# Kernel optimization log

Hardware: AMD Instinct MI355X
Metric: run time of the kernel (lower is better)

The kernel has to match this reference:

```python
import jax, jax.numpy as jnp
import numpy as np


def setup_inputs() -> dict:
    key = jax.random.key(0)
    ks = jax.random.split(key, 6)
    B, T, H, L, V = 8, 100, 1024, 512, 32000
    x = jax.random.normal(ks[0], (B, T, H), dtype=jnp.float32)
    attn_dist = jax.random.normal(ks[1], (B, T, L), dtype=jnp.float32)
    enc_input = jax.random.randint(ks[2], (B, L), 0, V, dtype=jnp.int32)
    W_vocab = jax.random.normal(ks[3], (H, V), dtype=jnp.float32) * (1.0 / np.sqrt(H))
    b_vocab = jnp.zeros((V,), dtype=jnp.float32)
    w_gen = jax.random.normal(ks[4], (H, 1), dtype=jnp.float32) * (1.0 / np.sqrt(H))
    b_gen = jnp.zeros((1,), dtype=jnp.float32)
    return {"x": x, "attn_dist": attn_dist, "enc_input": enc_input,
            "W_vocab": W_vocab, "b_vocab": b_vocab, "w_gen": w_gen, "b_gen": b_gen}


def reference(x, attn_dist, enc_input, W_vocab, b_vocab, w_gen, b_gen):
    B, T, H = x.shape
    L = attn_dist.shape[-1]
    V = W_vocab.shape[-1]
    # generation gate: sigmoid(x @ w_gen + b_gen) -> [B, T, 1]
    p_gen = jax.nn.sigmoid(jnp.einsum('bth,ho->bto', x, w_gen) + b_gen)
    # vocab distribution: softmax over vocab of the projection -> [B, T, V]
    vocab_dist = jax.nn.softmax(jnp.einsum('bth,hv->btv', x, W_vocab) + b_vocab, axis=-1)
    vocab_dist = p_gen * vocab_dist
    # copy distribution over encoder positions -> [B, T, L]
    copy_dist = (1.0 - p_gen) * jax.nn.softmax(attn_dist, axis=-1)
    # scatter-add copy probabilities into vocab slots (duplicates accumulate)
    vd = vocab_dist.reshape(B * T, V)
    cd = copy_dist.reshape(B * T, L)
    idx = jnp.broadcast_to(enc_input[:, None, :], (B, T, L)).reshape(B * T, L)
    rows = jnp.arange(B * T, dtype=jnp.int32)[:, None]
    combined = vd.at[rows, idx].add(cd)
    return jnp.log(combined).reshape(B, T, V)
```

## Files before the change

kernel.cpp:

```cpp
#include <hip/hip_runtime.h>
#include <math.h>

#define BB 8
#define TT 100
#define HH 1024
#define LL 512
#define VV 32000
#define NROWS (BB*TT)
#define MPAD 896
#define NMT 7
#define NNT 250
#define NWG (NMT*NNT)

typedef __bf16 bf16x8 __attribute__((ext_vector_type(8)));
typedef __bf16 bf16x4 __attribute__((ext_vector_type(4)));
typedef float f32x4 __attribute__((ext_vector_type(4)));

__device__ __forceinline__ void gload16(const void* g, void* l) {
  __builtin_amdgcn_global_load_lds(
      (const __attribute__((address_space(1))) unsigned int*)g,
      (__attribute__((address_space(3))) unsigned int*)l, 16, 0, 0);
}

__global__ __launch_bounds__(256) void k_cvt_x(const float* __restrict__ x,
                                               __bf16* __restrict__ xb) {
  int idx = blockIdx.x * 256 + threadIdx.x;
  int row = (idx * 4) >> 10;
  bf16x4 v;
  if (row < NROWS) {
    float4 f = ((const float4*)x)[idx];
    v[0] = (__bf16)f.x; v[1] = (__bf16)f.y; v[2] = (__bf16)f.z; v[3] = (__bf16)f.w;
  } else {
    v[0] = v[1] = v[2] = v[3] = (__bf16)0.f;
  }
  ((bf16x4*)xb)[idx] = v;
}

__global__ __launch_bounds__(256) void k_cvt_wT(const float* __restrict__ W,
                                                __bf16* __restrict__ Wtb) {
  __shared__ float T[32][257];
  int n0 = blockIdx.x * 256;
  int kt = blockIdx.y;
  int tid = threadIdx.x;
#pragma unroll
  for (int i = 0; i < 32; ++i)
    T[i][tid] = W[(size_t)(kt * 32 + i) * VV + n0 + tid];
  __syncthreads();
  int cq = tid & 3;
  int cl = tid >> 2;
  __bf16* base = Wtb + ((size_t)kt * VV + n0) * 32;
#pragma unroll
  for (int g = 0; g < 4; ++g) {
    int col = g * 64 + cl;
    bf16x8 v;
#pragma unroll
    for (int j = 0; j < 8; ++j) v[j] = (__bf16)T[cq * 8 + j][col];
    *(bf16x8*)(base + (size_t)col * 32 + cq * 8) = v;
  }
}

__global__ __launch_bounds__(256) void k_pgen_copy(
    const float* __restrict__ x, const float* __restrict__ attn,
    const float* __restrict__ w_gen, const float* __restrict__ b_gen,
    float* __restrict__ p_gen, float* __restrict__ copy_dist,
    float* __restrict__ rsum) {
  int r = blockIdx.x;
  int tid = threadIdx.x;
  __shared__ float red[4];
  if (tid == 0) rsum[r] = 0.f;

  float d = 0.f;
  for (int h = tid; h < HH; h += 256) d += x[(size_t)r * HH + h] * w_gen[h];
#pragma unroll
  for (int o = 32; o > 0; o >>= 1) d += __shfl_down(d, o, 64);
  if ((tid & 63) == 0) red[tid >> 6] = d;
  __syncthreads();
  float dot = red[0] + red[1] + red[2] + red[3];
  float p = 1.f / (1.f + __expf(-(dot + b_gen[0])));
  if (tid == 0) p_gen[r] = p;

  float a0 = attn[(size_t)r * LL + tid];
  float a1 = attn[(size_t)r * LL + 256 + tid];
  float m = fmaxf(a0, a1);
#pragma unroll
  for (int o = 32; o > 0; o >>= 1) m = fmaxf(m, __shfl_down(m, o, 64));
  __syncthreads();
  if ((tid & 63) == 0) red[tid >> 6] = m;
  __syncthreads();
  float M = fmaxf(fmaxf(red[0], red[1]), fmaxf(red[2], red[3]));
  float e0 = __expf(a0 - M), e1 = __expf(a1 - M);
  float s = e0 + e1;
#pragma unroll
  for (int o = 32; o > 0; o >>= 1) s += __shfl_down(s, o, 64);
  __syncthreads();
  if ((tid & 63) == 0) red[tid >> 6] = s;
  __syncthreads();
  float S = red[0] + red[1] + red[2] + red[3];
  float scale = (1.f - p) / S;
  copy_dist[(size_t)r * LL + tid] = e0 * scale;
  copy_dist[(size_t)r * LL + 256 + tid] = e1 * scale;
}

__global__ __launch_bounds__(256) void k_gemm_mfma(
    const __bf16* __restrict__ Xb, const __bf16* __restrict__ Wtb,
    const float* __restrict__ bias, float* __restrict__ out,
    float* __restrict__ rsum) {
  __shared__ __align__(16) __bf16 As[3][128 * 32];
  __shared__ __align__(16) __bf16 Bs[3][128 * 32];
  int tid = threadIdx.x;
  int lane = tid & 63, wave = tid >> 6;
  int wr = wave >> 1, wc = wave & 1;
  int l15 = lane & 15, quad = lane >> 4;

  int lid = blockIdx.x;
  int xcd = lid & 7, sub = lid >> 3;
  const int q = NWG >> 3, rr = NWG & 7;
  int wg = (xcd < rr) ? (xcd * (q + 1) + sub)
                      : (rr * (q + 1) + (xcd - rr) * q + sub);
  int m0 = (wg % NMT) * 128;
  int n0 = (wg / NMT) * 128;

  f32x4 acc[4][4];
#pragma unroll
  for (int mi = 0; mi < 4; ++mi)
#pragma unroll
    for (int ni = 0; ni < 4; ++ni) acc[mi][ni] = (f32x4){0.f, 0.f, 0.f, 0.f};

  int r0 = wave * 32;
  int lr = lane >> 2;
  int chunk = (lane & 3) ^ ((lr >> 1) & 3);
  const __bf16* aptr0 = Xb + (size_t)(m0 + r0 + lr) * HH + chunk * 8;
  const __bf16* aptr1 = aptr0 + (size_t)16 * HH;
  const size_t bstep = (size_t)VV * 32;
  const __bf16* bptr0 = Wtb + (size_t)(n0 + r0 + lr) * 32 + chunk * 8;
  const __bf16* bptr1 = bptr0 + (size_t)16 * 32;

  int sw8 = (quad ^ ((l15 >> 1) & 3)) * 8;

#define STAGE(it, buf) do {                                          \
    gload16(aptr0 + (size_t)(it) * 32, &As[buf][r0 * 32]);           \
    gload16(aptr1 + (size_t)(it) * 32, &As[buf][(r0 + 16) * 32]);    \
    gload16(bptr0 + (size_t)(it) * bstep, &Bs[buf][r0 * 32]);        \
    gload16(bptr1 + (size_t)(it) * bstep, &Bs[buf][(r0 + 16) * 32]); \
  } while (0)

#define SYNCW(n) do {                                          \
    asm volatile("s_waitcnt vmcnt(" #n ")" ::: "memory");      \
    __builtin_amdgcn_s_barrier();                              \
    __builtin_amdgcn_sched_barrier(0);                         \
  } while (0)

#define COMPUTE(buf) do {                                                     \
    const __bf16* Ab = As[buf];                                               \
    const __bf16* Bb = Bs[buf];                                               \
    bf16x8 af[4], bfg[4];                                                     \
    _Pragma("unroll")                                                         \
    for (int mi = 0; mi < 4; ++mi)                                            \
      af[mi] = *(const bf16x8*)&Ab[(wr * 64 + mi * 16 + l15) * 32 + sw8];     \
    _Pragma("unroll")                                                         \
    for (int ni = 0; ni < 4; ++ni)                                            \
      bfg[ni] = *(const bf16x8*)&Bb[(wc * 64 + ni * 16 + l15) * 32 + sw8];    \
    _Pragma("unroll")                                                         \
    for (int mi = 0; mi < 4; ++mi)                                            \
      _Pragma("unroll")                                                       \
      for (int ni = 0; ni < 4; ++ni)                                          \
        acc[mi][ni] = __builtin_amdgcn_mfma_f32_16x16x32_bf16(                \
            af[mi], bfg[ni], acc[mi][ni], 0, 0, 0);                           \
  } while (0)

  STAGE(0, 0);
  STAGE(1, 1);
  for (int itb = 0; itb < 30; itb += 3) {
    SYNCW(4); STAGE(itb + 2, 2); COMPUTE(0);
    SYNCW(4); STAGE(itb + 3, 0); COMPUTE(1);
    SYNCW(4); STAGE(itb + 4, 1); COMPUTE(2);
  }
  SYNCW(4);
  COMPUTE(0);
  SYNCW(0);
  COMPUTE(1);

  float bv4[4];
#pragma unroll
  for (int ni = 0; ni < 4; ++ni) bv4[ni] = bias[n0 + wc * 64 + ni * 16 + l15];

#pragma unroll
  for (int mi = 0; mi < 4; ++mi) {
#pragma unroll
    for (int rg = 0; rg < 4; ++rg) {
      int row = m0 + wr * 64 + mi * 16 + quad * 4 + rg;
      bool valid = row < NROWS;
      float esum = 0.f;
#pragma unroll
      for (int ni = 0; ni < 4; ++ni) {
        int col = n0 + wc * 64 + ni * 16 + l15;
        float v = acc[mi][ni][rg] + bv4[ni];
        if (valid) out[(size_t)row * VV + col] = v;
        esum += __expf(v);
      }
#pragma unroll
      for (int o = 8; o > 0; o >>= 1) esum += __shfl_down(esum, o, 16);
      if (l15 == 0 && valid) atomicAdd(&rsum[row], esum);
    }
  }
#undef STAGE
#undef SYNCW
#undef COMPUTE
}

__global__ __launch_bounds__(256) void k_affine_scatter(
    float* __restrict__ out, const float* __restrict__ p_gen,
    const float* __restrict__ rsum, const int* __restrict__ enc,
    const float* __restrict__ copy) {
  __shared__ int hkey[1024];
  __shared__ float hval[1024];
  int r = blockIdx.x, tid = threadIdx.x;
  float* row = out + (size_t)r * VV;
  float logc = __logf(p_gen[r] / rsum[r]);
  for (int i = tid; i < 1024; i += 256) { hkey[i] = -1; hval[i] = 0.f; }
  __syncthreads();
  int b = r / TT;
  for (int j = tid; j < LL; j += 256) {
    int v = enc[(size_t)b * LL + j];
    float cv = copy[(size_t)r * LL + j];
    unsigned h = ((unsigned)v * 2654435761u) & 1023u;
    while (true) {
      int prev = atomicCAS(&hkey[h], -1, v);
      if (prev == -1 || prev == v) { atomicAdd(&hval[h], cv); break; }
      h = (h + 1) & 1023u;
    }
  }
  for (int c4 = tid; c4 < VV / 4; c4 += 256) {
    float4 v = ((float4*)row)[c4];
    v.x += logc; v.y += logc; v.z += logc; v.w += logc;
    ((float4*)row)[c4] = v;
  }
  __syncthreads();
  for (int h = tid; h < 1024; h += 256) {
    int col = hkey[h];
    if (col >= 0) {
      float stored = row[col];
      row[col] = __logf(__expf(stored) + hval[h]);
    }
  }
}

extern "C" void kernel_launch(void* const* d_in, const int* in_sizes, int n_in,
                              void* d_out, int out_size, void* d_ws, size_t ws_size,
                              hipStream_t stream) {
  const float* x    = (const float*)d_in[0];
  const float* attn = (const float*)d_in[1];
  const int*   enc  = (const int*)d_in[2];
  const float* Wv   = (const float*)d_in[3];
  const float* bv   = (const float*)d_in[4];
  const float* wgen = (const float*)d_in[5];
  const float* bg   = (const float*)d_in[6];
  float* out = (float*)d_out;
  float* ws = (float*)d_ws;

  float* p_gen = ws;
  float* rsum  = ws + 1024;
  float* copy  = ws + 2048;
  __bf16* xb = (__bf16*)(ws + 2048 + NROWS * LL);
  __bf16* Wt = (__bf16*)((char*)xb + (size_t)MPAD * HH * 2);

  k_cvt_x<<<MPAD * HH / 4 / 256, 256, 0, stream>>>(x, xb);
  dim3 gw(VV / 256, HH / 32);
  k_cvt_wT<<<gw, 256, 0, stream>>>(Wv, Wt);
  k_pgen_copy<<<NROWS, 256, 0, stream>>>(x, attn, wgen, bg, p_gen, copy, rsum);
  k_gemm_mfma<<<NWG, 256, 0, stream>>>(xb, Wt, bv, out, rsum);
  k_affine_scatter<<<NROWS, 256, 0, stream>>>(out, p_gen, rsum, enc, copy);
}
```

Measured before the change: 405.9 us.

## Fuse W fp32-to-bf16 transpose into GEMM B-tile loading

Removes the separate kernel that converts and transposes W_vocab to bf16. The GEMM now loads fp32 W directly through registers, converts it and writes swizzled bf16 into LDS. The pipeline drops from three LDS buffers to two. This avoids a full extra read and write of the 128MB weight, but each of the 7 M-tiles now rereads fp32 W, doubling B bytes per tile, and loses the async direct-to-LDS path for B.

```diff
diff --git a/kernel.cpp b/kernel.cpp
--- a/kernel.cpp
+++ b/kernel.cpp
@@ -36,29 +36,6 @@
   ((bf16x4*)xb)[idx] = v;
 }
 
-__global__ __launch_bounds__(256) void k_cvt_wT(const float* __restrict__ W,
-                                                __bf16* __restrict__ Wtb) {
-  __shared__ float T[32][257];
-  int n0 = blockIdx.x * 256;
-  int kt = blockIdx.y;
-  int tid = threadIdx.x;
-#pragma unroll
-  for (int i = 0; i < 32; ++i)
-    T[i][tid] = W[(size_t)(kt * 32 + i) * VV + n0 + tid];
-  __syncthreads();
-  int cq = tid & 3;
-  int cl = tid >> 2;
-  __bf16* base = Wtb + ((size_t)kt * VV + n0) * 32;
-#pragma unroll
-  for (int g = 0; g < 4; ++g) {
-    int col = g * 64 + cl;
-    bf16x8 v;
-#pragma unroll
-    for (int j = 0; j < 8; ++j) v[j] = (__bf16)T[cq * 8 + j][col];
-    *(bf16x8*)(base + (size_t)col * 32 + cq * 8) = v;
-  }
-}
-
 __global__ __launch_bounds__(256) void k_pgen_copy(
     const float* __restrict__ x, const float* __restrict__ attn,
     const float* __restrict__ w_gen, const float* __restrict__ b_gen,
@@ -102,11 +79,11 @@
 }
 
 __global__ __launch_bounds__(256) void k_gemm_mfma(
-    const __bf16* __restrict__ Xb, const __bf16* __restrict__ Wtb,
+    const __bf16* __restrict__ Xb, const float* __restrict__ Wv,
     const float* __restrict__ bias, float* __restrict__ out,
     float* __restrict__ rsum) {
-  __shared__ __align__(16) __bf16 As[3][128 * 32];
-  __shared__ __align__(16) __bf16 Bs[3][128 * 32];
+  __shared__ __align__(16) __bf16 As[2][128 * 32];
+  __shared__ __align__(16) __bf16 Bs[2][128 * 32];
   int tid = threadIdx.x;
   int lane = tid & 63, wave = tid >> 6;
   int wr = wave >> 1, wc = wave & 1;
@@ -131,23 +108,39 @@
   int chunk = (lane & 3) ^ ((lr >> 1) & 3);
   const __bf16* aptr0 = Xb + (size_t)(m0 + r0 + lr) * HH + chunk * 8;
   const __bf16* aptr1 = aptr0 + (size_t)16 * HH;
-  const size_t bstep = (size_t)VV * 32;
-  const __bf16* bptr0 = Wtb + (size_t)(n0 + r0 + lr) * 32 + chunk * 8;
-  const __bf16* bptr1 = bptr0 + (size_t)16 * 32;
+  __bf16* lA0[2] = {&As[0][r0 * 32], &As[1][r0 * 32]};
+  __bf16* lA1[2] = {&As[0][(r0 + 16) * 32], &As[1][(r0 + 16) * 32]};
+
+  int nq = tid & 31;
+  int kb = tid >> 5;
+  const int rn0 = nq * 4;
+  const int bslot = (kb >> 1);
+  const int bsub = (kb & 1) * 4;
+  const float4* wsrc = (const float4*)Wv + (size_t)(kb * 4) * (VV / 4) + (n0 + nq * 4) / 4;
 
   int sw8 = (quad ^ ((l15 >> 1) & 3)) * 8;
 
-#define STAGE(it, buf) do {                                          \
-    gload16(aptr0 + (size_t)(it) * 32, &As[buf][r0 * 32]);           \
-    gload16(aptr1 + (size_t)(it) * 32, &As[buf][(r0 + 16) * 32]);    \
-    gload16(bptr0 + (size_t)(it) * bstep, &Bs[buf][r0 * 32]);        \
-    gload16(bptr1 + (size_t)(it) * bstep, &Bs[buf][(r0 + 16) * 32]); \
-  } while (0)
-
-#define SYNCW(n) do {                                          \
-    asm volatile("s_waitcnt vmcnt(" #n ")" ::: "memory");      \
-    __builtin_amdgcn_s_barrier();                              \
-    __builtin_amdgcn_sched_barrier(0);                         \
+#define STAGEA(it, buf) do {                        \
+    gload16(aptr0 + (size_t)(it) * 32, lA0[buf]);   \
+    gload16(aptr1 + (size_t)(it) * 32, lA1[buf]);   \
+  } while (0)
+
+#define LOADB(it) do {                                          \
+    _Pragma("unroll")                                           \
+    for (int jj = 0; jj < 4; ++jj)                              \
+      wv[jj] = wsrc[(size_t)((it) * 32 + jj) * (VV / 4)];       \
+  } while (0)
+
+#define WRITEB(buf) do {                                              \
+    _Pragma("unroll")                                                 \
+    for (int i = 0; i < 4; ++i) {                                     \
+      int rn = rn0 + i;                                               \
+      bf16x4 bv;                                                      \
+      bv[0] = (__bf16)wv[0][i]; bv[1] = (__bf16)wv[1][i];             \
+      bv[2] = (__bf16)wv[2][i]; bv[3] = (__bf16)wv[3][i];             \
+      int slot = bslot ^ ((rn >> 1) & 3);                             \
+      *(bf16x4*)&Bs[buf][rn * 32 + slot * 8 + bsub] = bv;             \
+    }                                                                 \
   } while (0)
 
 #define COMPUTE(buf) do {                                                     \
@@ -168,17 +161,22 @@
             af[mi], bfg[ni], acc[mi][ni], 0, 0, 0);                           \
   } while (0)
 
-  STAGE(0, 0);
-  STAGE(1, 1);
-  for (int itb = 0; itb < 30; itb += 3) {
-    SYNCW(4); STAGE(itb + 2, 2); COMPUTE(0);
-    SYNCW(4); STAGE(itb + 3, 0); COMPUTE(1);
-    SYNCW(4); STAGE(itb + 4, 1); COMPUTE(2);
-  }
-  SYNCW(4);
-  COMPUTE(0);
-  SYNCW(0);
-  COMPUTE(1);
+  float4 wv[4];
+  STAGEA(0, 0);
+  LOADB(0);
+  WRITEB(0);
+
+  for (int it = 0; it < 32; ++it) {
+    int cur = it & 1;
+    __syncthreads();
+    int nxt = cur ^ 1;
+    if (it + 1 < 32) {
+      STAGEA(it + 1, nxt);
+      LOADB(it + 1);
+    }
+    COMPUTE(cur);
+    if (it + 1 < 32) WRITEB(nxt);
+  }
 
   float bv4[4];
 #pragma unroll
@@ -203,8 +201,9 @@
       if (l15 == 0 && valid) atomicAdd(&rsum[row], esum);
     }
   }
-#undef STAGE
-#undef SYNCW
+#undef STAGEA
+#undef LOADB
+#undef WRITEB
 #undef COMPUTE
 }
 
@@ -262,12 +261,9 @@
   float* rsum  = ws + 1024;
   float* copy  = ws + 2048;
   __bf16* xb = (__bf16*)(ws + 2048 + NROWS * LL);
-  __bf16* Wt = (__bf16*)((char*)xb + (size_t)MPAD * HH * 2);
 
   k_cvt_x<<<MPAD * HH / 4 / 256, 256, 0, stream>>>(x, xb);
-  dim3 gw(VV / 256, HH / 32);
-  k_cvt_wT<<<gw, 256, 0, stream>>>(Wv, Wt);
   k_pgen_copy<<<NROWS, 256, 0, stream>>>(x, attn, wgen, bg, p_gen, copy, rsum);
-  k_gemm_mfma<<<NWG, 256, 0, stream>>>(xb, Wt, bv, out, rsum);
+  k_gemm_mfma<<<NWG, 256, 0, stream>>>(xb, Wv, bv, out, rsum);
   k_affine_scatter<<<NROWS, 256, 0, stream>>>(out, p_gen, rsum, enc, copy);
 }
```

Result: faster. 386.9 us (-4.7%).
